# Kernel tuning notes

Measured on AMD Instinct MI355X. Metric: run time of the kernel, lower is better.

The kernel has to match this reference:

```python
import jax, jax.numpy as jnp
import numpy as np
import math

SCOPE = 27
RICKER_WIDTH = 4.0
DAMP = 0.12
IN_CHANNELS = 128
BATCH, H, W = 64, 64, 64


def _mexican_hat(scope, std, damping):
    # Ricker (mexican hat) wavelet sampled on integer grid centered at scope//2,
    # matching weight_initialization.mexican_hat(scope, std, damping).
    x = np.arange(scope, dtype=np.float32) - scope // 2
    a = 2.0 / (np.sqrt(3.0 * std) * np.pi ** 0.25)
    wavelet = a * (1.0 - (x / std) ** 2) * np.exp(-(x ** 2) / (2.0 * std ** 2))
    return (damping * wavelet).astype(np.float32)


def setup_inputs() -> dict:
    key = jax.random.key(0)
    activations = jax.random.normal(key, (BATCH, IN_CHANNELS, H, W), dtype=jnp.float32)
    inhibition_filter = jnp.asarray(_mexican_hat(SCOPE, RICKER_WIDTH, DAMP)).reshape(1, 1, SCOPE)
    return {"activations": activations, "inhibition_filter": inhibition_filter}


def reference(activations, inhibition_filter):
    # activations: (N, C, H, W); inhibition_filter: (1, 1, scope)
    C = activations.shape[1]
    scope = inhibition_filter.shape[-1]

    # pad_roll: zero-pad filter to length C, roll so center lands at index 0 side
    pad_left = (C - scope) // 2
    pad_right = C - scope - pad_left
    k = jnp.concatenate([
        jnp.zeros((pad_left,), dtype=inhibition_filter.dtype),
        inhibition_filter[0, 0],
        jnp.zeros((pad_right,), dtype=inhibition_filter.dtype),
    ])
    k = jnp.roll(k, C // 2 + 1)  # (C,)

    # kronecker delta along channels
    delta = jnp.zeros((C,), dtype=activations.dtype).at[0].set(1.0)

    # frequency-domain deconvolution along the channel axis
    Fk = jnp.fft.fft(delta - k)  # (C,) complex
    sig = jnp.transpose(activations, (0, 2, 3, 1))  # NCHW -> NHWC
    out = jnp.fft.ifft(jnp.fft.fft(sig, axis=-1) / Fk, axis=-1).real
    return jnp.transpose(out, (0, 3, 1, 2)).astype(activations.dtype)
```

## Files before the change

### kernel.cpp

```cpp
#include <hip/hip_runtime.h>


typedef short bf16x8 __attribute__((ext_vector_type(8)));
typedef float f32x4 __attribute__((ext_vector_type(4)));

#define MFMA16x16x32 __builtin_amdgcn_mfma_f32_16x16x32_bf16

__device__ __forceinline__ unsigned short f2bf_rne(float f) {
  union { float f; unsigned u; } v; v.f = f;
  unsigned u = v.u;
  u += 0x7fffu + ((u >> 16) & 1u);
  return (unsigned short)(u >> 16);
}

__global__ void build_g(const float* __restrict__ filt,
                        unsigned short* __restrict__ gbf) {
  __shared__ float ct[128], st[128], fr[128], fi[128];
  const int t = threadIdx.x;
  const float ang = (float)t * 0.049087385212340526f;
  float s, c;
  __sincosf(ang, &s, &c);
  ct[t] = c; st[t] = s;
  __syncthreads();

  float re = 1.f, im = 0.f;
  for (int tt = 0; tt < 27; ++tt) {
    const int j = (115 + tt) & 127;
    const int idx = (j * t) & 127;
    const float kv = filt[tt];
    re -= kv * ct[idx];
    im += kv * st[idx];
  }
  fr[t] = re; fi[t] = im;
  __syncthreads();

  float acc = 0.f;
  for (int m = 0; m < 128; ++m) {
    const int idx = (m * t) & 127;
    const float dr = fr[m], di = fi[m];
    acc += (ct[idx] * dr + st[idx] * di) / (dr * dr + di * di);
  }
  gbf[t] = f2bf_rne(acc * (1.0f / 128.0f));
}

__global__ __launch_bounds__(256, 4) void conv_inhib(
    const float* __restrict__ X, const unsigned short* __restrict__ gtab,
    float* __restrict__ Y) {
  __shared__ __align__(16) unsigned short Xt[128 * 128];
  __shared__ unsigned short gsh[128];

  const int tid = threadIdx.x;
  const int l = tid & 63;
  const int w = tid >> 6;
  const int lane15 = l & 15;
  const int quad = l >> 4;

  const int bid = blockIdx.x;
  const int nimg = bid >> 5;
  const int s0 = (bid & 31) << 7;
  const float* Xn = X + (size_t)nimg * (128 * 4096);
  float* Yn = Y + (size_t)nimg * (128 * 4096);

  if (tid < 128) gsh[tid] = gtab[tid];

  {
    const int cb = tid & 7;
    const int sg = tid >> 3;
    const float* src = Xn + (size_t)(cb << 3) * 4096 + s0 + (sg << 2);
    f32x4 v[16];
#pragma unroll
    for (int p = 0; p < 2; ++p)
#pragma unroll
      for (int i = 0; i < 8; ++i)
        v[(p << 3) + i] = *(const f32x4*)(src + (size_t)((p << 6) + i) * 4096);
#pragma unroll
    for (int p = 0; p < 2; ++p) {
      const int chunk = cb + (p << 3);
#pragma unroll
      for (int j = 0; j < 4; ++j) {
        const int s = (sg << 2) + j;
        bf16x8 t;
#pragma unroll
        for (int i = 0; i < 8; ++i) t[i] = (short)f2bf_rne(v[(p << 3) + i][j]);
        *(bf16x8*)&Xt[(s << 7) + ((chunk ^ (s & 7)) << 3)] = t;
      }
    }
  }
  __syncthreads();

  bf16x8 bfrag[2][4];
#pragma unroll
  for (int nt = 0; nt < 2; ++nt) {
    const int cout = (w << 5) + (nt << 4) + lane15;
#pragma unroll
    for (int kk = 0; kk < 4; ++kk) {
      const int kb = (kk << 5) + (quad << 3);
#pragma unroll
      for (int j = 0; j < 8; ++j)
        bfrag[nt][kk][j] = (short)gsh[(cout - kb - j) & 127];
    }
  }

  f32x4 acc[8][2];
#pragma unroll
  for (int mt = 0; mt < 8; ++mt)
#pragma unroll
    for (int nt = 0; nt < 2; ++nt)
      acc[mt][nt] = (f32x4){0.f, 0.f, 0.f, 0.f};

#pragma unroll
  for (int mt = 0; mt < 8; ++mt) {
    const int srow = (mt << 4) + lane15;
    const int rb = srow << 7;
    const int sx = srow & 7;
#pragma unroll
    for (int kk = 0; kk < 4; ++kk) {
      const bf16x8 a = *(const bf16x8*)&Xt[rb + ((((kk << 2) + quad) ^ sx) << 3)];
      acc[mt][0] = MFMA16x16x32(a, bfrag[0][kk], acc[mt][0], 0, 0, 0);
      acc[mt][1] = MFMA16x16x32(a, bfrag[1][kk], acc[mt][1], 0, 0, 0);
    }
  }

#pragma unroll
  for (int nt = 0; nt < 2; ++nt) {
    const int c = (w << 5) + (nt << 4) + lane15;
    float* Yc = Yn + (size_t)c * 4096 + s0 + (quad << 2);
#pragma unroll
    for (int mt = 0; mt < 8; ++mt) {
      *(f32x4*)(Yc + (mt << 4)) = acc[mt][nt];
    }
  }
}

extern "C" void kernel_launch(void* const* d_in, const int* in_sizes, int n_in,
                              void* d_out, int out_size, void* d_ws, size_t ws_size,
                              hipStream_t stream) {
  const float* act = (const float*)d_in[0];
  const float* filt = (const float*)d_in[1];
  float* out = (float*)d_out;
  unsigned short* g = (unsigned short*)d_ws;

  build_g<<<1, 128, 0, stream>>>(filt, g);
  conv_inhib<<<2048, 256, 0, stream>>>(act, g, out);
}
```

Before: 246.5 us.

## Load activations straight into MFMA registers, drop LDS staging, exploit circulant filter

```diff
diff --git a/kernel.cpp b/kernel.cpp
--- a/kernel.cpp
+++ b/kernel.cpp
@@ -43,12 +43,9 @@
   gbf[t] = f2bf_rne(acc * (1.0f / 128.0f));
 }
 
-__global__ __launch_bounds__(256, 4) void conv_inhib(
+__global__ __launch_bounds__(256, 3) void conv_inhib(
     const float* __restrict__ X, const unsigned short* __restrict__ gtab,
     float* __restrict__ Y) {
-  __shared__ __align__(16) unsigned short Xt[128 * 128];
-  __shared__ unsigned short gsh[128];
-
   const int tid = threadIdx.x;
   const int l = tid & 63;
   const int w = tid >> 6;
@@ -56,78 +53,61 @@
   const int quad = l >> 4;
 
   const int bid = blockIdx.x;
-  const int nimg = bid >> 5;
-  const int s0 = (bid & 31) << 7;
+  const int nimg = bid >> 4;
+  const int sw = ((bid & 15) << 8) + (w << 6);
   const float* Xn = X + (size_t)nimg * (128 * 4096);
   float* Yn = Y + (size_t)nimg * (128 * 4096);
 
-  if (tid < 128) gsh[tid] = gtab[tid];
+  bf16x8 U[8];
+#pragma unroll
+  for (int t = 0; t < 8; ++t) {
+    const int base = (t << 4) + lane15 - (quad << 3);
+#pragma unroll
+    for (int j = 0; j < 8; ++j)
+      U[t][j] = (short)gtab[(base - j) & 127];
+  }
 
-  {
-    const int cb = tid & 7;
-    const int sg = tid >> 3;
-    const float* src = Xn + (size_t)(cb << 3) * 4096 + s0 + (sg << 2);
-    f32x4 v[16];
+  const float* colbase = Xn + sw + lane15;
+  const int rowoff = (quad << 3);
+
+  float raw[32];
 #pragma unroll
-    for (int p = 0; p < 2; ++p)
+  for (int kk = 0; kk < 4; ++kk)
 #pragma unroll
-      for (int i = 0; i < 8; ++i)
-        v[(p << 3) + i] = *(const f32x4*)(src + (size_t)((p << 6) + i) * 4096);
+    for (int j = 0; j < 8; ++j)
+      raw[(kk << 3) + j] = colbase[(size_t)((kk << 5) + rowoff + j) * 4096];
+
 #pragma unroll
-    for (int p = 0; p < 2; ++p) {
-      const int chunk = cb + (p << 3);
+  for (int t = 0; t < 4; ++t) {
+    bf16x8 af[4];
 #pragma unroll
-      for (int j = 0; j < 4; ++j) {
-        const int s = (sg << 2) + j;
-        bf16x8 t;
-#pragma unroll
-        for (int i = 0; i < 8; ++i) t[i] = (short)f2bf_rne(v[(p << 3) + i][j]);
-        *(bf16x8*)&Xt[(s << 7) + ((chunk ^ (s & 7)) << 3)] = t;
-      }
-    }
-  }
-  __syncthreads();
-
-  bf16x8 bfrag[2][4];
-#pragma unroll
-  for (int nt = 0; nt < 2; ++nt) {
-    const int cout = (w << 5) + (nt << 4) + lane15;
-#pragma unroll
-    for (int kk = 0; kk < 4; ++kk) {
-      const int kb = (kk << 5) + (quad << 3);
+    for (int kk = 0; kk < 4; ++kk)
 #pragma unroll
       for (int j = 0; j < 8; ++j)
-        bfrag[nt][kk][j] = (short)gsh[(cout - kb - j) & 127];
+        af[kk][j] = (short)f2bf_rne(raw[(kk << 3) + j]);
+
+    if (t < 3) {
+      const float* nb = colbase + ((t + 1) << 4);
+#pragma unroll
+      for (int kk = 0; kk < 4; ++kk)
+#pragma unroll
+        for (int j = 0; j < 8; ++j)
+          raw[(kk << 3) + j] = nb[(size_t)((kk << 5) + rowoff + j) * 4096];
     }
-  }
 
-  f32x4 acc[8][2];
+    f32x4 acc[8];
 #pragma unroll
-  for (int mt = 0; mt < 8; ++mt)
+    for (int nt = 0; nt < 8; ++nt) acc[nt] = (f32x4){0.f, 0.f, 0.f, 0.f};
 #pragma unroll
-    for (int nt = 0; nt < 2; ++nt)
-      acc[mt][nt] = (f32x4){0.f, 0.f, 0.f, 0.f};
+    for (int nt = 0; nt < 8; ++nt)
+#pragma unroll
+      for (int kk = 0; kk < 4; ++kk)
+        acc[nt] = MFMA16x16x32(af[kk], U[(nt - 2 * kk) & 7], acc[nt], 0, 0, 0);
 
+    const int scol = sw + (t << 4) + (quad << 2);
 #pragma unroll
-  for (int mt = 0; mt < 8; ++mt) {
-    const int srow = (mt << 4) + lane15;
-    const int rb = srow << 7;
-    const int sx = srow & 7;
-#pragma unroll
-    for (int kk = 0; kk < 4; ++kk) {
-      const bf16x8 a = *(const bf16x8*)&Xt[rb + ((((kk << 2) + quad) ^ sx) << 3)];
-      acc[mt][0] = MFMA16x16x32(a, bfrag[0][kk], acc[mt][0], 0, 0, 0);
-      acc[mt][1] = MFMA16x16x32(a, bfrag[1][kk], acc[mt][1], 0, 0, 0);
-    }
-  }
-
-#pragma unroll
-  for (int nt = 0; nt < 2; ++nt) {
-    const int c = (w << 5) + (nt << 4) + lane15;
-    float* Yc = Yn + (size_t)c * 4096 + s0 + (quad << 2);
-#pragma unroll
-    for (int mt = 0; mt < 8; ++mt) {
-      *(f32x4*)(Yc + (mt << 4)) = acc[mt][nt];
+    for (int nt = 0; nt < 8; ++nt) {
+      *(f32x4*)(Yn + (size_t)((nt << 4) + lane15) * 4096 + scol) = acc[nt];
     }
   }
 }
@@ -141,5 +121,5 @@
   unsigned short* g = (unsigned short*)d_ws;
 
   build_g<<<1, 128, 0, stream>>>(filt, g);
-  conv_inhib<<<2048, 256, 0, stream>>>(act, g, out);
+  conv_inhib<<<1024, 256, 0, stream>>>(act, g, out);
 }
```

After: 322.4 us. 30.8% more time.

## Double spatial tile per block, use 512 threads, load filter fragments from global

Applied to the files above, without the earlier changes.

```diff
diff --git a/kernel.cpp b/kernel.cpp
--- a/kernel.cpp
+++ b/kernel.cpp
@@ -11,6 +11,10 @@
   unsigned u = v.u;
   u += 0x7fffu + ((u >> 16) & 1u);
   return (unsigned short)(u >> 16);
+}
+
+__device__ __forceinline__ int lds_key(int s) {
+  return (s & 7) ^ ((s >> 3) & 7);
 }
 
 __global__ void build_g(const float* __restrict__ filt,
@@ -43,91 +47,77 @@
   gbf[t] = f2bf_rne(acc * (1.0f / 128.0f));
 }
 
-__global__ __launch_bounds__(256, 4) void conv_inhib(
+__global__ __launch_bounds__(512, 4) void conv_inhib(
     const float* __restrict__ X, const unsigned short* __restrict__ gtab,
     float* __restrict__ Y) {
-  __shared__ __align__(16) unsigned short Xt[128 * 128];
-  __shared__ unsigned short gsh[128];
+  __shared__ __align__(16) unsigned short Xt[256 * 128];
 
   const int tid = threadIdx.x;
-  const int l = tid & 63;
+  const int t = tid & 63;
   const int w = tid >> 6;
-  const int lane15 = l & 15;
-  const int quad = l >> 4;
+  const int lane15 = t & 15;
+  const int quad = t >> 4;
 
   const int bid = blockIdx.x;
-  const int nimg = bid >> 5;
-  const int s0 = (bid & 31) << 7;
+  const int nimg = bid >> 4;
+  const int s0 = (bid & 15) << 8;
   const float* Xn = X + (size_t)nimg * (128 * 4096);
   float* Yn = Y + (size_t)nimg * (128 * 4096);
 
-  if (tid < 128) gsh[tid] = gtab[tid];
+  f32x4 v[16];
+  {
+    const float* base = Xn + (size_t)(w << 4) * 4096 + s0 + (t << 2);
+#pragma unroll
+    for (int i = 0; i < 16; ++i)
+      v[i] = *(const f32x4*)(base + (size_t)i * 4096);
+  }
 
-  {
-    const int cb = tid & 7;
-    const int sg = tid >> 3;
-    const float* src = Xn + (size_t)(cb << 3) * 4096 + s0 + (sg << 2);
-    f32x4 v[16];
+  const int cout = (w << 4) + lane15;
+  bf16x8 U[4];
 #pragma unroll
-    for (int p = 0; p < 2; ++p)
+  for (int kk = 0; kk < 4; ++kk) {
+    const int kb = cout - (kk << 5) - (quad << 3);
 #pragma unroll
-      for (int i = 0; i < 8; ++i)
-        v[(p << 3) + i] = *(const f32x4*)(src + (size_t)((p << 6) + i) * 4096);
+    for (int j = 0; j < 8; ++j)
+      U[kk][j] = (short)gtab[(kb - j) & 127];
+  }
+
 #pragma unroll
-    for (int p = 0; p < 2; ++p) {
-      const int chunk = cb + (p << 3);
+  for (int b = 0; b < 2; ++b) {
+    const int oct = (w << 1) + b;
 #pragma unroll
-      for (int j = 0; j < 4; ++j) {
-        const int s = (sg << 2) + j;
-        bf16x8 t;
+    for (int j = 0; j < 4; ++j) {
+      const int s = (t << 2) + j;
+      bf16x8 q;
 #pragma unroll
-        for (int i = 0; i < 8; ++i) t[i] = (short)f2bf_rne(v[(p << 3) + i][j]);
-        *(bf16x8*)&Xt[(s << 7) + ((chunk ^ (s & 7)) << 3)] = t;
-      }
+      for (int i = 0; i < 8; ++i) q[i] = (short)f2bf_rne(v[(b << 3) + i][j]);
+      *(bf16x8*)&Xt[(s << 7) + ((oct ^ lds_key(s)) << 3)] = q;
     }
   }
   __syncthreads();
 
-  bf16x8 bfrag[2][4];
+  f32x4 acc[16];
 #pragma unroll
-  for (int nt = 0; nt < 2; ++nt) {
-    const int cout = (w << 5) + (nt << 4) + lane15;
+  for (int mt = 0; mt < 16; ++mt) acc[mt] = (f32x4){0.f, 0.f, 0.f, 0.f};
+
+#pragma unroll
+  for (int mt = 0; mt < 16; ++mt) {
+    const int srow = (mt << 4) + lane15;
+    const int key = lds_key(srow);
+    const int rb = srow << 7;
 #pragma unroll
     for (int kk = 0; kk < 4; ++kk) {
-      const int kb = (kk << 5) + (quad << 3);
-#pragma unroll
-      for (int j = 0; j < 8; ++j)
-        bfrag[nt][kk][j] = (short)gsh[(cout - kb - j) & 127];
+      const int oct = (kk << 2) + quad;
+      const bf16x8 a = *(const bf16x8*)&Xt[rb + ((oct ^ key) << 3)];
+      acc[mt] = MFMA16x16x32(a, U[kk], acc[mt], 0, 0, 0);
     }
   }
 
-  f32x4 acc[8][2];
+  {
+    float* Yc = Yn + (size_t)cout * 4096 + s0 + (quad << 2);
 #pragma unroll
-  for (int mt = 0; mt < 8; ++mt)
-#pragma unroll
-    for (int nt = 0; nt < 2; ++nt)
-      acc[mt][nt] = (f32x4){0.f, 0.f, 0.f, 0.f};
-
-#pragma unroll
-  for (int mt = 0; mt < 8; ++mt) {
-    const int srow = (mt << 4) + lane15;
-    const int rb = srow << 7;
-    const int sx = srow & 7;
-#pragma unroll
-    for (int kk = 0; kk < 4; ++kk) {
-      const bf16x8 a = *(const bf16x8*)&Xt[rb + ((((kk << 2) + quad) ^ sx) << 3)];
-      acc[mt][0] = MFMA16x16x32(a, bfrag[0][kk], acc[mt][0], 0, 0, 0);
-      acc[mt][1] = MFMA16x16x32(a, bfrag[1][kk], acc[mt][1], 0, 0, 0);
-    }
-  }
-
-#pragma unroll
-  for (int nt = 0; nt < 2; ++nt) {
-    const int c = (w << 5) + (nt << 4) + lane15;
-    float* Yc = Yn + (size_t)c * 4096 + s0 + (quad << 2);
-#pragma unroll
-    for (int mt = 0; mt < 8; ++mt) {
-      *(f32x4*)(Yc + (mt << 4)) = acc[mt][nt];
+    for (int mt = 0; mt < 16; ++mt) {
+      *(f32x4*)(Yc + (mt << 4)) = acc[mt];
     }
   }
 }
@@ -141,5 +131,5 @@
   unsigned short* g = (unsigned short*)d_ws;
 
   build_g<<<1, 128, 0, stream>>>(filt, g);
-  conv_inhib<<<2048, 256, 0, stream>>>(act, g, out);
+  conv_inhib<<<1024, 512, 0, stream>>>(act, g, out);
 }
```

After: 249.3 us. About the same (+1.1%).
